# Kernel optimization log

Hardware: AMD Instinct MI355X
Metric: run time of the kernel (lower is better)

Reference implementation:

```python
import jax, jax.numpy as jnp
import numpy as np
from jax import lax

GAMMA = 1.0
BIG = 1e8  # matches the torch init value 100000000.0


def setup_inputs() -> dict:
    key = jax.random.key(0)
    k1, k2 = jax.random.split(key)
    B, n, m, d = 256, 256, 256, 32
    x = jax.random.normal(k1, (B, n, d), dtype=jnp.float32)
    y = jax.random.normal(k2, (B, m, d), dtype=jnp.float32)
    return {"x": x, "y": y}


def _soft_dtw(x, y, gamma):
    B, n, d = x.shape
    m = y.shape[1]
    # squared euclidean distances, (B, n, m); GEMM form avoids the (B,n,m,d) blowup
    x2 = jnp.sum(x * x, axis=-1)
    y2 = jnp.sum(y * y, axis=-1)
    dist = x2[:, :, None] + y2[:, None, :] - 2.0 * jnp.einsum('bnd,bmd->bnm', x, y)
    dist = jnp.maximum(dist, 0.0)  # cdist(p=2)**2 is nonnegative

    def softmin3(a, b, c):
        s = jnp.stack([a, b, c], axis=0)
        return -gamma * jax.nn.logsumexp(-s / gamma, axis=0)

    big_col = jnp.full((B,), BIG, dtype=x.dtype)

    def row_step(prev_row, d_row):
        # prev_row: (B, m+1) = D[i-1, :];  d_row: (B, m) = dist[:, i-1, :]
        def col_step(cur, inp):
            # cur: (B,) = D[i, j-1]; inp: (dist[i-1,j-1], D[i-1,j], D[i-1,j-1])
            dij, up, diag = inp
            new = dij + softmin3(up, cur, diag)
            return new, new
        xs = (d_row.T, prev_row[:, 1:].T, prev_row[:, :-1].T)  # each (m, B)
        _, vals = lax.scan(col_step, big_col, xs)  # vals: (m, B)
        new_row = jnp.concatenate([big_col[:, None], vals.T], axis=1)  # (B, m+1)
        return new_row, None

    init_row = jnp.concatenate(
        [jnp.zeros((B, 1), x.dtype), jnp.full((B, m), BIG, dtype=x.dtype)], axis=1)
    final_row, _ = lax.scan(row_step, init_row, jnp.swapaxes(dist, 0, 1))  # scan over n rows
    return jnp.mean(final_row[:, m])


def reference(x, y):
    return _soft_dtw(x, y, GAMMA)
```

## Files before the change

### kernel.cpp

```cpp
#include <hip/hip_runtime.h>

#define BIG 1e8f
#define LN2 0.69314718f
#define LOG2E 1.44269504f
#define M2L -2.8853900818f

#define RSLOT 112
#define DRB 1040

#define OFF_XH   116480
#define OFF_X2S  132864
#define OFF_Y2S  133888
#define OFF_RDY  134912
#define OFF_PRG  134976
#define LDS_BYTES 135040

typedef _Float16 half8 __attribute__((ext_vector_type(8)));
typedef _Float16 half2_t __attribute__((ext_vector_type(2)));
typedef float f32x4 __attribute__((ext_vector_type(4)));

__device__ __forceinline__ float exp2g(float x) {
#if __has_builtin(__builtin_amdgcn_exp2f)
    return __builtin_amdgcn_exp2f(x);
#else
    return exp2f(x);
#endif
}
__device__ __forceinline__ float log2g(float x) {
#if __has_builtin(__builtin_amdgcn_logf)
    return __builtin_amdgcn_logf(x);
#else
    return log2f(x);
#endif
}

__device__ __forceinline__ half2_t pkrtz(float a, float b) {
    return __builtin_bit_cast(half2_t, __builtin_amdgcn_cvt_pkrtz(a, b));
}


__device__ __forceinline__ void pmerge(float Ma, float Sa, float Mb, float Sb,
                                       float& Mo, float& So) {
    const float d = Ma - Mb;
    const float e = exp2g(-fabsf(d));
    Mo = fminf(Ma, Mb);
    So = (d <= 0.f) ? fmaf(Sb, e, Sa) : fmaf(Sa, e, Sb);
}

__device__ __forceinline__ void pcell(float Mm, float Sm, float Mv, float Sv,
                                      float dd, float& Mo, float& So) {
    const float dlt = Mv - Mm;
    const float e = exp2g(-fabsf(dlt));
    const float mu = fminf(Mm, Mv);
    So = (dlt >= 0.f) ? fmaf(Sv, e, Sm) : fmaf(Sm, e, Sv);
    Mo = dd + mu;
}

__device__ __forceinline__ float shfl_up1(float v, float oldv) {
    int r = __builtin_amdgcn_update_dpp(
        __builtin_bit_cast(int, oldv), __builtin_bit_cast(int, v),
        0x138 , 0xf, 0xf, false);
    return __builtin_bit_cast(float, r);
}

__device__ __forceinline__ void dec2(unsigned int w, float& a, float& b) {
    half2_t h = __builtin_bit_cast(half2_t, w);
    a = (float)h[0];
    b = (float)h[1];
}

#define MASKW0 0x7BFF7BFFu
#define MASKW1 0x70007000u
#define MASKW2 0x60006000u
#define MASKW3 0x50005000u

__global__ __launch_bounds__(128, 1) void sdtw_kernel(
    const float* __restrict__ x, const float* __restrict__ y,
    float* __restrict__ out) {
    extern __shared__ __align__(16) char smem[];
    unsigned char* band = (unsigned char*)smem;
    _Float16* xh = (_Float16*)(smem + OFF_XH);
    float* x2sL = (float*)(smem + OFF_X2S);
    float* y2sL = (float*)(smem + OFF_Y2S);
    volatile int* rdy = (volatile int*)(smem + OFF_RDY);
    volatile int* prg = (volatile int*)(smem + OFF_PRG);

    const int tid = threadIdx.x;
    const int b = blockIdx.x;
    const float* xb = x + (size_t)b * 8192;
    const float* yb = y + (size_t)b * 8192;

#pragma unroll
    for (int rr = 0; rr < 2; rr++) {
        const int r = tid + rr * 128;
        const float4* px = (const float4*)(xb + r * 32);
        union { _Float16 h[32]; half8 v[4]; } uc;
        float s2 = 0.f;
#pragma unroll
        for (int q = 0; q < 8; q++) {
            float4 f = px[q];
            s2 += f.x * f.x + f.y * f.y + f.z * f.z + f.w * f.w;
            uc.h[4 * q + 0] = (_Float16)f.x;
            uc.h[4 * q + 1] = (_Float16)f.y;
            uc.h[4 * q + 2] = (_Float16)f.z;
            uc.h[4 * q + 3] = (_Float16)f.w;
        }
        half8* dst = (half8*)&xh[r * 32];
#pragma unroll
        for (int q = 0; q < 4; q++) dst[q] = uc.v[q];
        x2sL[r] = s2 * LOG2E;

        const float4* py = (const float4*)(yb + r * 32);
        float t2 = 0.f;
#pragma unroll
        for (int q = 0; q < 8; q++) {
            float4 f = py[q];
            t2 += f.x * f.x + f.y * f.y + f.z * f.z + f.w * f.w;
        }
        y2sL[r] = t2 * LOG2E;
    }
    if (tid < 16) rdy[tid] = 0;
    if (tid == 16) *prg = 0;
    __syncthreads();

    if (tid >= 64) {
        const int lane = tid - 64;
        const int qd = lane >> 4, xr = lane & 15;

        half8 yfrag[16];
        float yvL[16];
#pragma unroll
        for (int ci = 0; ci < 16; ci++) {
            const float* yp = yb + (ci * 16 + xr) * 32 + qd * 8;
            float4 f0 = *(const float4*)yp;
            float4 f1 = *(const float4*)(yp + 4);
            half8 v;
            v[0] = (_Float16)f0.x; v[1] = (_Float16)f0.y;
            v[2] = (_Float16)f0.z; v[3] = (_Float16)f0.w;
            v[4] = (_Float16)f1.x; v[5] = (_Float16)f1.y;
            v[6] = (_Float16)f1.z; v[7] = (_Float16)f1.w;
            yfrag[ci] = v;
            yvL[ci] = y2sL[ci * 16 + xr];
        }

        for (int sg = 0; sg < 16; sg++) {
            if (sg >= 6) {
                const int need = 8 * sg - 40;
                while (*prg < need) {}
            }
            const half8 xf = *(const half8*)&xh[(sg * 16 + xr) * 32 + qd * 8];
            const float4 xl = *(const float4*)&x2sL[sg * 16 + qd * 4];
            const int p0 = 8 * sg + 2 * qd;
#pragma unroll
            for (int ci = 0; ci < 16; ci++) {
                f32x4 acc = {0.f, 0.f, 0.f, 0.f};
                acc = __builtin_amdgcn_mfma_f32_16x16x32_f16(xf, yfrag[ci], acc, 0, 0, 0);
                const int c = ci * 16 + xr;
                const float yv = yvL[ci];
                const float d0 = fmaxf(fmaf(M2L, acc[0], xl.x + yv), 0.f);
                const float d1 = fmaxf(fmaf(M2L, acc[1], xl.y + yv), 0.f);
                const float d2 = fmaxf(fmaf(M2L, acc[2], xl.z + yv), 0.f);
                const float d3 = fmaxf(fmaf(M2L, acc[3], xl.w + yv), 0.f);
                const half2_t h01 = pkrtz(d0, d1);
                const half2_t h23 = pkrtz(d2, d3);
                const int dr0 = p0 + (c >> 2);
                int s0_ = dr0;     if (s0_ >= RSLOT) s0_ -= RSLOT;
                int s1_ = dr0 + 1; if (s1_ >= RSLOT) s1_ -= RSLOT;
                *(half2_t*)&band[s0_ * DRB + 4 * c] = h01;
                *(half2_t*)&band[s1_ * DRB + 4 * c] = h23;
            }
            __threadfence_block();
            if (lane == 0) rdy[sg] = 1;
        }
        return;
    }

    const int lane = tid;
    float MpA3 = BIG, SpA3 = 1.f, MpB3 = BIG, SpB3 = 1.f;
    float MG0 = (lane == 0) ? 0.f : BIG, SG0 = 1.f;
    float Mm0, Sm0, Mm1, Sm1, Mm2, Sm2, Mm3, Sm3;
    pmerge(BIG, 1.f, MG0, SG0, Mm0, Sm0);
    pmerge(BIG, 1.f, BIG, 1.f, Mm1, Sm1);
    Mm2 = Mm1; Sm2 = Sm1;
    Mm3 = Mm1; Sm3 = Sm1;

    while (rdy[0] == 0) {}
    uint4 wreg = *(const uint4*)&band[16 * lane];

    auto step = [&](int s_) {
        const float MLA = shfl_up1(MpA3, BIG);
        const float SLA = shfl_up1(SpA3, 1.f);
        const float MLB = shfl_up1(MpB3, BIG);
        const float SLB = shfl_up1(SpB3, 1.f);

        const bool act = (unsigned)(s_ - lane - 1) < 128u;
        const unsigned wx = act ? wreg.x : MASKW0;
        const unsigned wy = act ? wreg.y : MASKW1;
        const unsigned wz = act ? wreg.z : MASKW2;
        const unsigned ww = act ? wreg.w : MASKW3;
        float dA0, dB0, dA1, dB1, dA2, dB2, dA3, dB3;
        dec2(wx, dA0, dB0);
        dec2(wy, dA1, dB1);
        dec2(wz, dA2, dB2);
        dec2(ww, dA3, dB3);

        int dn = (s_ > 190) ? 190 : s_;
        if (dn >= RSLOT) dn -= RSLOT;
        const uint4 wnext = *(const uint4*)&band[dn * DRB + 16 * lane];

        float MA0, SA0, MA1, SA1, MA2, SA2, MA3, SA3;
        pcell(Mm0, Sm0, MLA, SLA, dA0, MA0, SA0);
        pcell(Mm1, Sm1, MA0, SA0, dA1, MA1, SA1);
        pcell(Mm2, Sm2, MA1, SA1, dA2, MA2, SA2);
        pcell(Mm3, Sm3, MA2, SA2, dA3, MA3, SA3);

        float Mn0, Sn0, Mn1, Sn1, Mn2, Sn2, Mn3, Sn3;
        pmerge(MA0, SA0, MLA, SLA, Mn0, Sn0);
        pmerge(MA1, SA1, MA0, SA0, Mn1, Sn1);
        pmerge(MA2, SA2, MA1, SA1, Mn2, Sn2);
        pmerge(MA3, SA3, MA2, SA2, Mn3, Sn3);
        float MB0, SB0, MB1, SB1, MB2, SB2, MB3, SB3;
        pcell(Mn0, Sn0, MLB, SLB, dB0, MB0, SB0);
        pcell(Mn1, Sn1, MB0, SB0, dB1, MB1, SB1);
        pcell(Mn2, Sn2, MB1, SB1, dB2, MB2, SB2);
        pcell(Mn3, Sn3, MB2, SB2, dB3, MB3, SB3);

        MpA3 = MA3; SpA3 = SA3;
        MpB3 = MB3; SpB3 = SB3;
        MG0 = MLB; SG0 = SLB;
        pmerge(MB0, SB0, MG0, SG0, Mm0, Sm0);
        pmerge(MB1, SB1, MB0, SB0, Mm1, Sm1);
        pmerge(MB2, SB2, MB1, SB1, Mm2, Sm2);
        pmerge(MB3, SB3, MB2, SB2, Mm3, Sm3);
        wreg = wnext;
    };

#pragma unroll
    for (int s_ = 1; s_ < 8; s_++) step(s_);

    for (int g = 1; g < 24; g++) {
        int st = (g > 15) ? 15 : g;
        while (rdy[st] == 0) {}
        if (lane == 0) *prg = 8 * g;
        const int s0 = 8 * g;
#pragma unroll
        for (int k = 0; k < 8; k++) step(s0 + k);
    }

    if (lane == 63)
        atomicAdd(out, (MpB3 - log2g(SpB3)) * (LN2 / 256.f));
}

extern "C" void kernel_launch(void* const* d_in, const int* in_sizes, int n_in,
                              void* d_out, int out_size, void* d_ws, size_t ws_size,
                              hipStream_t stream) {
    const float* x = (const float*)d_in[0];
    const float* y = (const float*)d_in[1];
    float* out = (float*)d_out;
    const int B = in_sizes[0] / (256 * 32);

    (void)hipFuncSetAttribute((const void*)sdtw_kernel,
                              hipFuncAttributeMaxDynamicSharedMemorySize,
                              LDS_BYTES);
    (void)hipMemsetAsync(d_out, 0, sizeof(float), stream);
    sdtw_kernel<<<dim3(B), dim3(128), LDS_BYTES, stream>>>(x, y, out);
}
```

Before: 130.0 us.

## Decouple max-tracking chain from sum chain in soft-DTW wavefront step

Restructures the per-step log-sum-exp recurrence so the running-minimum (M) chain is computed first, with all exp2 arguments taken as mu minus each input instead of -|delta|. All exponentials are then issued together, and the scale (S) chain becomes a pure FMA/multiply recurrence. This shortens the serial dependency through transcendental ops and lets exp2 calls overlap. The cost is two exp2 per merge instead of one, and more live registers.

```diff
diff --git a/kernel.cpp b/kernel.cpp
--- a/kernel.cpp
+++ b/kernel.cpp
@@ -36,24 +36,6 @@
 
 __device__ __forceinline__ half2_t pkrtz(float a, float b) {
     return __builtin_bit_cast(half2_t, __builtin_amdgcn_cvt_pkrtz(a, b));
-}
-
-
-__device__ __forceinline__ void pmerge(float Ma, float Sa, float Mb, float Sb,
-                                       float& Mo, float& So) {
-    const float d = Ma - Mb;
-    const float e = exp2g(-fabsf(d));
-    Mo = fminf(Ma, Mb);
-    So = (d <= 0.f) ? fmaf(Sb, e, Sa) : fmaf(Sa, e, Sb);
-}
-
-__device__ __forceinline__ void pcell(float Mm, float Sm, float Mv, float Sv,
-                                      float dd, float& Mo, float& So) {
-    const float dlt = Mv - Mm;
-    const float e = exp2g(-fabsf(dlt));
-    const float mu = fminf(Mm, Mv);
-    So = (dlt >= 0.f) ? fmaf(Sv, e, Sm) : fmaf(Sm, e, Sv);
-    Mo = dd + mu;
 }
 
 __device__ __forceinline__ float shfl_up1(float v, float oldv) {
@@ -177,20 +159,20 @@
 
     const int lane = tid;
     float MpA3 = BIG, SpA3 = 1.f, MpB3 = BIG, SpB3 = 1.f;
-    float MG0 = (lane == 0) ? 0.f : BIG, SG0 = 1.f;
-    float Mm0, Sm0, Mm1, Sm1, Mm2, Sm2, Mm3, Sm3;
-    pmerge(BIG, 1.f, MG0, SG0, Mm0, Sm0);
-    pmerge(BIG, 1.f, BIG, 1.f, Mm1, Sm1);
-    Mm2 = Mm1; Sm2 = Sm1;
-    Mm3 = Mm1; Sm3 = Sm1;
+    float Mm[4], Sm[4];
+    Mm[0] = (lane == 0) ? 0.f : BIG;
+    Sm[0] = (lane == 0) ? 1.f : 2.f;
+    Mm[1] = BIG; Sm[1] = 2.f;
+    Mm[2] = BIG; Sm[2] = 2.f;
+    Mm[3] = BIG; Sm[3] = 2.f;
 
     while (rdy[0] == 0) {}
     uint4 wreg = *(const uint4*)&band[16 * lane];
 
     auto step = [&](int s_) {
         const float MLA = shfl_up1(MpA3, BIG);
+        const float MLB = shfl_up1(MpB3, BIG);
         const float SLA = shfl_up1(SpA3, 1.f);
-        const float MLB = shfl_up1(MpB3, BIG);
         const float SLB = shfl_up1(SpB3, 1.f);
 
         const bool act = (unsigned)(s_ - lane - 1) < 128u;
@@ -198,40 +180,100 @@
         const unsigned wy = act ? wreg.y : MASKW1;
         const unsigned wz = act ? wreg.z : MASKW2;
         const unsigned ww = act ? wreg.w : MASKW3;
-        float dA0, dB0, dA1, dB1, dA2, dB2, dA3, dB3;
-        dec2(wx, dA0, dB0);
-        dec2(wy, dA1, dB1);
-        dec2(wz, dA2, dB2);
-        dec2(ww, dA3, dB3);
+        float dA[4], dB[4];
+        dec2(wx, dA[0], dB[0]);
+        dec2(wy, dA[1], dB[1]);
+        dec2(wz, dA[2], dB[2]);
+        dec2(ww, dA[3], dB[3]);
 
         int dn = (s_ > 190) ? 190 : s_;
         if (dn >= RSLOT) dn -= RSLOT;
         const uint4 wnext = *(const uint4*)&band[dn * DRB + 16 * lane];
 
-        float MA0, SA0, MA1, SA1, MA2, SA2, MA3, SA3;
-        pcell(Mm0, Sm0, MLA, SLA, dA0, MA0, SA0);
-        pcell(Mm1, Sm1, MA0, SA0, dA1, MA1, SA1);
-        pcell(Mm2, Sm2, MA1, SA1, dA2, MA2, SA2);
-        pcell(Mm3, Sm3, MA2, SA2, dA3, MA3, SA3);
-
-        float Mn0, Sn0, Mn1, Sn1, Mn2, Sn2, Mn3, Sn3;
-        pmerge(MA0, SA0, MLA, SLA, Mn0, Sn0);
-        pmerge(MA1, SA1, MA0, SA0, Mn1, Sn1);
-        pmerge(MA2, SA2, MA1, SA1, Mn2, Sn2);
-        pmerge(MA3, SA3, MA2, SA2, Mn3, Sn3);
-        float MB0, SB0, MB1, SB1, MB2, SB2, MB3, SB3;
-        pcell(Mn0, Sn0, MLB, SLB, dB0, MB0, SB0);
-        pcell(Mn1, Sn1, MB0, SB0, dB1, MB1, SB1);
-        pcell(Mn2, Sn2, MB1, SB1, dB2, MB2, SB2);
-        pcell(Mn3, Sn3, MB2, SB2, dB3, MB3, SB3);
-
-        MpA3 = MA3; SpA3 = SA3;
-        MpB3 = MB3; SpB3 = SB3;
-        MG0 = MLB; SG0 = SLB;
-        pmerge(MB0, SB0, MG0, SG0, Mm0, Sm0);
-        pmerge(MB1, SB1, MB0, SB0, Mm1, Sm1);
-        pmerge(MB2, SB2, MB1, SB1, Mm2, Sm2);
-        pmerge(MB3, SB3, MB2, SB2, Mm3, Sm3);
+        float MA[4], xAm[4], xAv[4];
+        float prevA = MLA;
+#pragma unroll
+        for (int k = 0; k < 4; k++) {
+            const float mu = fminf(Mm[k], prevA);
+            xAm[k] = mu - Mm[k];
+            xAv[k] = mu - prevA;
+            MA[k] = dA[k] + mu;
+            prevA = MA[k];
+        }
+        float muN[4], xNa[4], xNb[4];
+        float diagA = MLA;
+#pragma unroll
+        for (int k = 0; k < 4; k++) {
+            muN[k] = fminf(MA[k], diagA);
+            xNa[k] = muN[k] - MA[k];
+            xNb[k] = muN[k] - diagA;
+            diagA = MA[k];
+        }
+        float MB[4], xBm[4], xBv[4];
+        float prevB = MLB;
+#pragma unroll
+        for (int k = 0; k < 4; k++) {
+            const float mu = fminf(muN[k], prevB);
+            xBm[k] = mu - muN[k];
+            xBv[k] = mu - prevB;
+            MB[k] = dB[k] + mu;
+            prevB = MB[k];
+        }
+        float muC[4], xCa[4], xCb[4];
+        float diagB = MLB;
+#pragma unroll
+        for (int k = 0; k < 4; k++) {
+            muC[k] = fminf(MB[k], diagB);
+            xCa[k] = muC[k] - MB[k];
+            xCb[k] = muC[k] - diagB;
+            diagB = MB[k];
+        }
+
+        float eAm[4], eAv[4], eNa[4], eNb[4], eBm[4], eBv[4], eCa[4], eCb[4];
+#pragma unroll
+        for (int k = 0; k < 4; k++) {
+            eAm[k] = exp2g(xAm[k]);
+            eAv[k] = exp2g(xAv[k]);
+            eNa[k] = exp2g(xNa[k]);
+            eNb[k] = exp2g(xNb[k]);
+            eBm[k] = exp2g(xBm[k]);
+            eBv[k] = exp2g(xBv[k]);
+            eCa[k] = exp2g(xCa[k]);
+            eCb[k] = exp2g(xCb[k]);
+        }
+
+        float SA[4];
+        float ps = SLA;
+#pragma unroll
+        for (int k = 0; k < 4; k++) {
+            SA[k] = fmaf(Sm[k], eAm[k], ps * eAv[k]);
+            ps = SA[k];
+        }
+        float SN[4];
+        float dsg = SLA;
+#pragma unroll
+        for (int k = 0; k < 4; k++) {
+            SN[k] = fmaf(SA[k], eNa[k], dsg * eNb[k]);
+            dsg = SA[k];
+        }
+        float SB[4];
+        ps = SLB;
+#pragma unroll
+        for (int k = 0; k < 4; k++) {
+            SB[k] = fmaf(SN[k], eBm[k], ps * eBv[k]);
+            ps = SB[k];
+        }
+        dsg = SLB;
+#pragma unroll
+        for (int k = 0; k < 4; k++) {
+            Sm[k] = fmaf(SB[k], eCa[k], dsg * eCb[k]);
+            dsg = SB[k];
+        }
+
+        MpA3 = MA[3]; SpA3 = SA[3];
+        MpB3 = MB[3]; SpB3 = SB[3];
+#pragma unroll
+        for (int k = 0; k < 4; k++) Mm[k] = muC[k];
         wreg = wnext;
     };
 
```

New measurement: 134.8 us. 3.7% more time.
